# Kernel tuning notes

Measured on AMD Instinct MI355X. Metric: run time of the kernel, lower is better.

## Reference

```python
import jax, jax.numpy as jnp
import numpy as np

N = 100000
E = 3200000
IN_DIM = 500
HID = 64
OUT_DIM = 40
K = 10
ALPHA = 0.1
BN_EPS = 1e-5


def setup_inputs() -> dict:
    key = jax.random.key(0)
    ks = jax.random.split(key, 10)
    x = jax.random.normal(ks[0], (N, IN_DIM), dtype=jnp.float32)
    edge_index = jax.random.randint(ks[1], (2, E), 0, N, dtype=jnp.int64)
    W1 = jax.random.normal(ks[2], (IN_DIM, HID), dtype=jnp.float32) / np.sqrt(IN_DIM)
    b1 = jnp.zeros((HID,), dtype=jnp.float32)
    bn_gamma = jnp.ones((HID,), dtype=jnp.float32)
    bn_beta = jnp.zeros((HID,), dtype=jnp.float32)
    bn_mean = jax.random.normal(ks[3], (HID,), dtype=jnp.float32) * 0.1
    bn_var = jax.random.uniform(ks[4], (HID,), dtype=jnp.float32) + 0.5
    W2 = jax.random.normal(ks[5], (HID, OUT_DIM), dtype=jnp.float32) / np.sqrt(HID)
    b2 = jnp.zeros((OUT_DIM,), dtype=jnp.float32)
    return {"x": x, "edge_index": edge_index, "W1": W1, "b1": b1,
            "bn_gamma": bn_gamma, "bn_beta": bn_beta, "bn_mean": bn_mean,
            "bn_var": bn_var, "W2": W2, "b2": b2}


def _gcn_norm(edge_index):
    # PyG gcn_norm with add_self_loops=True, symmetric normalization.
    row = jnp.concatenate([edge_index[0], jnp.arange(N, dtype=edge_index.dtype)])
    col = jnp.concatenate([edge_index[1], jnp.arange(N, dtype=edge_index.dtype)])
    deg = jax.ops.segment_sum(jnp.ones_like(col, dtype=jnp.float32), col, num_segments=N)
    dinv = jnp.where(deg > 0, jax.lax.rsqrt(deg), 0.0)
    norm = dinv[row] * dinv[col]  # [E+N]
    return row, col, norm


def _appnp(x, row, col, norm):
    h = x
    def step(xk, _):
        msg = norm[:, None] * xk[row]                       # [E+N, HID] gather
        agg = jax.ops.segment_sum(msg, col, num_segments=N)  # scatter-add
        return (1.0 - ALPHA) * agg + ALPHA * h, None
    xK, _ = jax.lax.scan(step, x, None, length=K)
    return xK


def reference(x, edge_index, W1, b1, bn_gamma, bn_beta, bn_mean, bn_var, W2, b2):
    row, col, norm = _gcn_norm(edge_index)
    h = x @ W1 + b1                                   # lin1
    h = _appnp(h, row, col, norm)                     # K-step APPNP
    h = (h - bn_mean) * jax.lax.rsqrt(bn_var + BN_EPS) * bn_gamma + bn_beta  # BN (eval)
    # dropout is identity in eval mode
    emb = h @ W2 + b2                                 # lin2
    out = jax.nn.log_softmax(emb, axis=1)
    return out, emb
```

## Files before the change

kernel.cpp:

```cpp
#include <hip/hip_runtime.h>
#include <math.h>

#define N_NODES 100000
#define N_EDGES 3200000
#define IN_DIM  500
#define HID     64
#define OUT_DIM 40
#define K_ITERS 10
#define ALPHA   0.1f
#define BN_EPS  1e-5f

#define WPAD 48
#define YD   40
#define YH   20
#define NBUCK 782
#define TILE_A 8192
#define APG 48

__device__ __forceinline__ void unpack8(uint4 v, float f[8]) {
    f[0] = __uint_as_float(v.x << 16);
    f[1] = __uint_as_float(v.x & 0xffff0000u);
    f[2] = __uint_as_float(v.y << 16);
    f[3] = __uint_as_float(v.y & 0xffff0000u);
    f[4] = __uint_as_float(v.z << 16);
    f[5] = __uint_as_float(v.z & 0xffff0000u);
    f[6] = __uint_as_float(v.w << 16);
    f[7] = __uint_as_float(v.w & 0xffff0000u);
}
__device__ __forceinline__ unsigned pack2(float a, float b) {
    unsigned ua = __float_as_uint(a);
    unsigned ub = __float_as_uint(b);
    ua += ((ua >> 16) & 1u) + 0x7fffu;
    ub += ((ub >> 16) & 1u) + 0x7fffu;
    return (ua >> 16) | (ub & 0xffff0000u);
}
__device__ __forceinline__ float edge_w(unsigned e) {
    return __uint_as_float((e >> 17) << 16);
}
__device__ __forceinline__ void fma8(float acc[8], float wgt, const float f[8]) {
#pragma unroll
    for (int i = 0; i < 8; ++i) acc[i] = fmaf(wgt, f[i], acc[i]);
}


__global__ void zero_cnt_kernel(int* __restrict__ cnt) {
    int i = blockIdx.x * 256 + threadIdx.x;
    if (i < N_NODES) cnt[i] = 0;
}

__global__ void hist_kernel(const int* __restrict__ ei, int* __restrict__ cnt) {
    int e = blockIdx.x * 256 + threadIdx.x;
    if (e < N_EDGES) atomicAdd(&cnt[ei[N_EDGES + e]], 1);
}

__global__ void reduce_kernel(const int* __restrict__ cnt, int* __restrict__ psum) {
    __shared__ int s[256];
    int i = blockIdx.x * 256 + threadIdx.x;
    int v = (i < N_NODES) ? cnt[i] : 0;
    s[threadIdx.x] = v;
    __syncthreads();
    for (int off = 128; off > 0; off >>= 1) {
        if (threadIdx.x < (unsigned)off) s[threadIdx.x] += s[threadIdx.x + off];
        __syncthreads();
    }
    if (threadIdx.x == 0) psum[blockIdx.x] = s[0];
}

__global__ void scanp_kernel(const int* __restrict__ psum, int* __restrict__ pexcl,
                             int nparts) {
    __shared__ int s[512];
    int t = threadIdx.x;
    int v = (t < nparts) ? psum[t] : 0;
    s[t] = v;
    __syncthreads();
    for (int off = 1; off < 512; off <<= 1) {
        int tv = (t >= off) ? s[t - off] : 0;
        __syncthreads();
        s[t] += tv;
        __syncthreads();
    }
    if (t < nparts) pexcl[t] = s[t] - v;
}

__global__ void apply_kernel(const int* __restrict__ cnt, const int* __restrict__ pexcl,
                             int* __restrict__ rowptr, float* __restrict__ dinv) {
    __shared__ int s[256];
    int t = threadIdx.x;
    int i = blockIdx.x * 256 + t;
    int v = (i < N_NODES) ? cnt[i] : 0;
    s[t] = v;
    __syncthreads();
    for (int off = 1; off < 256; off <<= 1) {
        int tv = (t >= off) ? s[t - off] : 0;
        __syncthreads();
        s[t] += tv;
        __syncthreads();
    }
    if (i < N_NODES) {
        int excl = pexcl[blockIdx.x] + s[t] - v;
        rowptr[i] = excl;
        dinv[i] = rsqrtf((float)(v + 1));
        if (i == N_NODES - 1) rowptr[N_NODES] = excl + v;
    }
}


__global__ void bcur_init_kernel(const int* __restrict__ rowptr, int* __restrict__ bcursor) {
    int i = blockIdx.x * 256 + threadIdx.x;
    if (i < NBUCK) bcursor[i] = rowptr[i << 7];
}

__global__ __launch_bounds__(256) void bucketA_kernel(const int* __restrict__ ei,
                                                      int* __restrict__ bcursor,
                                                      unsigned* __restrict__ ebuf) {
    __shared__ int cnt[NBUCK];
    __shared__ int gbase[NBUCK];
    for (int i = threadIdx.x; i < NBUCK; i += 256) cnt[i] = 0;
    __syncthreads();
    const int e0 = blockIdx.x * TILE_A;
    const int e1 = (e0 + TILE_A < N_EDGES) ? e0 + TILE_A : N_EDGES;
    for (int e = e0 + threadIdx.x; e < e1; e += 256)
        atomicAdd(&cnt[ei[N_EDGES + e] >> 7], 1);
    __syncthreads();
    for (int i = threadIdx.x; i < NBUCK; i += 256) {
        int n = cnt[i];
        gbase[i] = (n > 0) ? atomicAdd(&bcursor[i], n) : 0;
        cnt[i] = 0;
    }
    __syncthreads();
    for (int e = e0 + threadIdx.x; e < e1; e += 256) {
        int r = ei[e];
        int c = ei[N_EDGES + e];
        int b = c >> 7;
        int rank = atomicAdd(&cnt[b], 1);
        ebuf[gbase[b] + rank] = (unsigned)r | ((unsigned)(c & 127) << 17);
    }
}

__global__ __launch_bounds__(256) void bucketB_kernel(const unsigned* __restrict__ ebuf,
                                                      const int* __restrict__ rowptr,
                                                      const float* __restrict__ dinv,
                                                      unsigned* __restrict__ ew) {
    __shared__ int lcur[128];
    __shared__ float ldinv[128];
    const int base = blockIdx.x << 7;
    const int nn = (N_NODES - base < 128) ? (N_NODES - base) : 128;
    if (threadIdx.x < (unsigned)nn) {
        lcur[threadIdx.x] = rowptr[base + threadIdx.x];
        ldinv[threadIdx.x] = dinv[base + threadIdx.x];
    }
    __syncthreads();
    const int s0 = rowptr[base];
    const int hi = (base + 128 < N_NODES) ? base + 128 : N_NODES;
    const int s1 = rowptr[hi];
    for (int p = s0 + threadIdx.x; p < s1; p += 256) {
        unsigned v = ebuf[p];
        int r = v & 0x1ffff;
        int cl = v >> 17;
        int pos = atomicAdd(&lcur[cl], 1);
        float w = dinv[r] * ldinv[cl];
        unsigned f = __float_as_uint(w) + 0x8000u;
        ew[pos] = (unsigned)r | ((f >> 16) << 17);
    }
}

__global__ void prep_kernel(const float* __restrict__ W2, const float* __restrict__ gamma,
                            const float* __restrict__ beta, const float* __restrict__ mean,
                            const float* __restrict__ var, const float* __restrict__ b1,
                            const float* __restrict__ b2, float* __restrict__ W2p,
                            float* __restrict__ c1, float* __restrict__ cbeta) {
    __shared__ float sc[64];
    __shared__ float sd[64];
    int t = threadIdx.x;
    if (t < 64) {
        float s = rsqrtf(var[t] + BN_EPS) * gamma[t];
        sc[t] = s;
        sd[t] = beta[t] - mean[t] * s;
    }
    __syncthreads();
    for (int i = t; i < 64 * OUT_DIM; i += 256) {
        int f = i / OUT_DIM;
        W2p[i] = sc[f] * W2[i];
    }
    if (t < WPAD) {
        if (t < OUT_DIM) {
            float acb = b2[t], ac1 = 0.f;
            for (int f = 0; f < 64; ++f) {
                float w2 = W2[f * OUT_DIM + t];
                acb = fmaf(sd[f], w2, acb);
                ac1 = fmaf(b1[f] * sc[f], w2, ac1);
            }
            cbeta[t] = acb;
            c1[t] = ac1;
        } else {
            c1[t] = 0.f;
        }
    }
}

__global__ __launch_bounds__(256) void wc_kernel(const float* __restrict__ W1,
                                                 const float* __restrict__ W2p,
                                                 float* __restrict__ Wc) {
    __shared__ float w2s[64 * OUT_DIM];
    for (int i = threadIdx.x; i < 64 * OUT_DIM; i += 256) w2s[i] = W2p[i];
    __syncthreads();
    int idx = blockIdx.x * 256 + threadIdx.x;
    if (idx >= IN_DIM * WPAD) return;
    int k = idx / WPAD, o = idx % WPAD;
    float a = 0.f;
    if (o < OUT_DIM) {
        const float* w1r = W1 + (size_t)k * HID;
#pragma unroll 8
        for (int f = 0; f < 64; ++f) a = fmaf(w1r[f], w2s[f * OUT_DIM + o], a);
    }
    Wc[idx] = a;
}

#define L1_M  128
#define L1_KC 20
#define L1_PITCH 132
__global__ __launch_bounds__(256) void lin1_kernel(const float* __restrict__ x,
                                                   const float* __restrict__ Wc,
                                                   const float* __restrict__ c1,
                                                   float* __restrict__ y0f,
                                                   unsigned* __restrict__ y0b) {
    __shared__ float xsT[L1_KC * L1_PITCH];
    __shared__ float wcs[L1_KC * WPAD];

    const int t = threadIdx.x;
    const int ng = t & 31;
    const int og = t >> 5;
    const int nbase = blockIdx.x * L1_M;

    const int srow = t >> 1;
    const int skb  = (t & 1) * 10;
    const int gsrc = nbase + srow;
    const int gcl  = (gsrc < N_NODES) ? gsrc : (N_NODES - 1);
    const float* xrow = x + (size_t)gcl * IN_DIM;

    float acc[4][6];
#pragma unroll
    for (int i = 0; i < 4; ++i)
#pragma unroll
        for (int j = 0; j < 6; ++j) acc[i][j] = 0.0f;

    for (int k0 = 0; k0 < IN_DIM; k0 += L1_KC) {
        __syncthreads();
#pragma unroll
        for (int u = 0; u < 5; ++u) {
            const float2 xv = *(const float2*)(xrow + k0 + skb + 2 * u);
            xsT[(skb + 2 * u) * L1_PITCH + srow]     = xv.x;
            xsT[(skb + 2 * u + 1) * L1_PITCH + srow] = xv.y;
        }
        for (int i = t; i < L1_KC * WPAD; i += 256) wcs[i] = Wc[(size_t)k0 * WPAD + i];
        __syncthreads();

#pragma unroll 4
        for (int k = 0; k < L1_KC; ++k) {
            const float4 xv = *(const float4*)&xsT[k * L1_PITCH + ng * 4];
            float w[6];
#pragma unroll
            for (int j = 0; j < 6; ++j) w[j] = wcs[k * WPAD + og * 6 + j];
            const float xr[4] = {xv.x, xv.y, xv.z, xv.w};
#pragma unroll
            for (int i = 0; i < 4; ++i)
#pragma unroll
                for (int j = 0; j < 6; ++j)
                    acc[i][j] = fmaf(xr[i], w[j], acc[i][j]);
        }
    }

    float cc[6];
#pragma unroll
    for (int j = 0; j < 6; ++j) cc[j] = c1[og * 6 + j];
#pragma unroll
    for (int i = 0; i < 4; ++i) {
        const int n = nbase + ng * 4 + i;
        if (n < N_NODES) {
            float o[6];
#pragma unroll
            for (int j = 0; j < 6; ++j) o[j] = acc[i][j] + cc[j];
            float* yf = y0f + (size_t)n * YD + og * 6;
            unsigned* yb = y0b + (size_t)n * YH + og * 3;
            if (og < 6) {
                *(float2*)(yf)     = make_float2(o[0], o[1]);
                *(float2*)(yf + 2) = make_float2(o[2], o[3]);
                *(float2*)(yf + 4) = make_float2(o[4], o[5]);
                yb[0] = pack2(o[0], o[1]);
                yb[1] = pack2(o[2], o[3]);
                yb[2] = pack2(o[4], o[5]);
            } else if (og == 6) {
                *(float2*)(yf)     = make_float2(o[0], o[1]);
                *(float2*)(yf + 2) = make_float2(o[2], o[3]);
                yb[0] = pack2(o[0], o[1]);
                yb[1] = pack2(o[2], o[3]);
            }
        }
    }
}

template <bool LAST>
__global__ __launch_bounds__(256) void appnp40_kernel(const int* __restrict__ rowptr,
                                                      const unsigned* __restrict__ ew,
                                                      const float* __restrict__ dinv,
                                                      const unsigned* __restrict__ yin,
                                                      const float* __restrict__ h,
                                                      unsigned* __restrict__ yout,
                                                      float* __restrict__ yKf) {
    const int wv   = threadIdx.x >> 6;
    const int lane = threadIdx.x & 63;
    const int sub  = lane / 5;
    const int dl   = lane - sub * 5;
    const int node = blockIdx.x * APG + wv * 12 + sub;
    const bool act = (lane < 60) && (node < N_NODES);
    const int dl4  = dl * 4;

    int beg = 0, end = 0;
    float selfw = 0.f;
    if (act) {
        beg = rowptr[node];
        end = rowptr[node + 1];
        const float di = dinv[node];
        selfw = di * di;
    }

    uint4 vs = make_uint4(0, 0, 0, 0);
    float4 h0 = make_float4(0.f, 0.f, 0.f, 0.f), h1 = h0;
    if (act) {
        vs = *(const uint4*)(yin + (size_t)node * YH + dl4);
        h0 = *(const float4*)(h + (size_t)node * YD + dl * 8);
        h1 = *(const float4*)(h + (size_t)node * YD + dl * 8 + 4);
    }

    float acc[8];
#pragma unroll
    for (int i = 0; i < 8; ++i) acc[i] = 0.f;

    int p = beg;
    for (; p + 3 < end; p += 4) {
        const unsigned e0 = ew[p], e1 = ew[p + 1], e2 = ew[p + 2], e3 = ew[p + 3];
        const uint4 v0 = *(const uint4*)(yin + (size_t)(e0 & 0x1ffff) * YH + dl4);
        const uint4 v1 = *(const uint4*)(yin + (size_t)(e1 & 0x1ffff) * YH + dl4);
        const uint4 v2 = *(const uint4*)(yin + (size_t)(e2 & 0x1ffff) * YH + dl4);
        const uint4 v3 = *(const uint4*)(yin + (size_t)(e3 & 0x1ffff) * YH + dl4);
        float f[8];
        unpack8(v0, f); fma8(acc, edge_w(e0), f);
        unpack8(v1, f); fma8(acc, edge_w(e1), f);
        unpack8(v2, f); fma8(acc, edge_w(e2), f);
        unpack8(v3, f); fma8(acc, edge_w(e3), f);
    }
    for (; p < end; ++p) {
        const unsigned e0 = ew[p];
        const uint4 v0 = *(const uint4*)(yin + (size_t)(e0 & 0x1ffff) * YH + dl4);
        float f[8];
        unpack8(v0, f);
        fma8(acc, edge_w(e0), f);
    }

    if (act) {
        float fs[8];
        unpack8(vs, fs);
        const float ha[8] = {h0.x, h0.y, h0.z, h0.w, h1.x, h1.y, h1.z, h1.w};
        float o[8];
#pragma unroll
        for (int i = 0; i < 8; ++i)
            o[i] = (1.0f - ALPHA) * fmaf(selfw, fs[i], acc[i]) + ALPHA * ha[i];
        if (LAST) {
            *(float4*)(yKf + (size_t)node * YD + dl * 8)     = make_float4(o[0], o[1], o[2], o[3]);
            *(float4*)(yKf + (size_t)node * YD + dl * 8 + 4) = make_float4(o[4], o[5], o[6], o[7]);
        } else {
            uint4 w;
            w.x = pack2(o[0], o[1]);
            w.y = pack2(o[2], o[3]);
            w.z = pack2(o[4], o[5]);
            w.w = pack2(o[6], o[7]);
            *(uint4*)(yout + (size_t)node * YH + dl4) = w;
        }
    }
}

__global__ __launch_bounds__(256) void final_kernel(const float* __restrict__ yKf,
                                                    const float* __restrict__ cbeta,
                                                    float* __restrict__ out_ls,
                                                    float* __restrict__ out_emb) {
    const int lane = threadIdx.x & 63;
    const int wv   = threadIdx.x >> 6;
    const int node = blockIdx.x * 4 + wv;

    float e = 0.0f;
    if (lane < OUT_DIM) e = yKf[(size_t)node * YD + lane] + cbeta[lane];
    float ev = (lane < OUT_DIM) ? e : -INFINITY;
    float m = ev;
#pragma unroll
    for (int off = 32; off > 0; off >>= 1) m = fmaxf(m, __shfl_xor(m, off, 64));
    float p = (lane < OUT_DIM) ? expf(ev - m) : 0.0f;
    float s = p;
#pragma unroll
    for (int off = 32; off > 0; off >>= 1) s += __shfl_xor(s, off, 64);
    if (lane < OUT_DIM) {
        float ls = ev - m - logf(s);
        out_ls[(size_t)node * OUT_DIM + lane] = ls;
        out_emb[(size_t)node * OUT_DIM + lane] = e;
    }
}


extern "C" void kernel_launch(void* const* d_in, const int* in_sizes, int n_in,
                              void* d_out, int out_size, void* d_ws, size_t ws_size,
                              hipStream_t stream) {
    const float* x     = (const float*)d_in[0];
    const int*   ei    = (const int*)d_in[1];
    const float* W1    = (const float*)d_in[2];
    const float* b1    = (const float*)d_in[3];
    const float* gamma = (const float*)d_in[4];
    const float* beta  = (const float*)d_in[5];
    const float* mean  = (const float*)d_in[6];
    const float* var   = (const float*)d_in[7];
    const float* W2    = (const float*)d_in[8];
    const float* b2    = (const float*)d_in[9];

    char* ws = (char*)d_ws;
    size_t off = 0;
    auto alloc = [&](size_t bytes) { char* p = ws + off; off += (bytes + 255) & ~(size_t)255; return p; };

    unsigned* ew     = (unsigned*)alloc((size_t)N_EDGES * 4);
    unsigned* ebuf   = (unsigned*)alloc((size_t)N_EDGES * 4);
    float*    y0f    = (float*)   alloc((size_t)N_NODES * YD * 4);
    float*    yKf    = (float*)   alloc((size_t)N_NODES * YD * 4);
    unsigned* y0b    = (unsigned*)alloc((size_t)N_NODES * YH * 4);
    unsigned* ya     = (unsigned*)alloc((size_t)N_NODES * YH * 4);
    unsigned* yb     = (unsigned*)alloc((size_t)N_NODES * YH * 4);
    float*    Wc     = (float*)   alloc((size_t)IN_DIM * WPAD * 4);
    float*    W2p    = (float*)   alloc(64 * OUT_DIM * 4);
    float*    c1     = (float*)   alloc(WPAD * 4);
    float*    cbeta  = (float*)   alloc(OUT_DIM * 4);
    int*      cnt    = (int*)     alloc(N_NODES * 4);
    float*    dinv   = (float*)   alloc(N_NODES * 4);
    int*      rowptr = (int*)     alloc((N_NODES + 1) * 4);
    int*      bcursor= (int*)     alloc(NBUCK * 4);
    int*      psum   = (int*)     alloc(1600 * 4);
    int*      pexcl  = (int*)     alloc(1600 * 4);

    float* out_ls  = (float*)d_out;
    float* out_emb = (float*)d_out + (size_t)N_NODES * OUT_DIM;

    const int NB_N = (N_NODES + 255) / 256;
    const int NB_E = (N_EDGES + 255) / 256;
    const int NB_A = (N_EDGES + TILE_A - 1) / TILE_A;
    const int NB_P = (N_NODES + APG - 1) / APG;

    zero_cnt_kernel<<<NB_N, 256, 0, stream>>>(cnt);
    hist_kernel<<<NB_E, 256, 0, stream>>>(ei, cnt);
    reduce_kernel<<<NB_N, 256, 0, stream>>>(cnt, psum);
    scanp_kernel<<<1, 512, 0, stream>>>(psum, pexcl, NB_N);
    apply_kernel<<<NB_N, 256, 0, stream>>>(cnt, pexcl, rowptr, dinv);
    bcur_init_kernel<<<(NBUCK + 255) / 256, 256, 0, stream>>>(rowptr, bcursor);
    bucketA_kernel<<<NB_A, 256, 0, stream>>>(ei, bcursor, ebuf);
    bucketB_kernel<<<NBUCK, 256, 0, stream>>>(ebuf, rowptr, dinv, ew);

    prep_kernel<<<1, 256, 0, stream>>>(W2, gamma, beta, mean, var, b1, b2, W2p, c1, cbeta);
    wc_kernel<<<(IN_DIM * WPAD + 255) / 256, 256, 0, stream>>>(W1, W2p, Wc);
    lin1_kernel<<<(N_NODES + L1_M - 1) / L1_M, 256, 0, stream>>>(x, Wc, c1, y0f, y0b);

    const unsigned* cur = y0b;
    unsigned* nxt = ya;
    unsigned* buf[2] = {ya, yb};
    for (int k = 0; k < K_ITERS - 1; ++k) {
        appnp40_kernel<false><<<NB_P, 256, 0, stream>>>(rowptr, ew, dinv, cur,
                                                        y0f, nxt, nullptr);
        cur = nxt;
        nxt = buf[(k + 1) & 1];
    }
    appnp40_kernel<true><<<NB_P, 256, 0, stream>>>(rowptr, ew, dinv, cur,
                                                   y0f, nullptr, yKf);

    final_kernel<<<N_NODES / 4, 256, 0, stream>>>(yKf, cbeta, out_ls, out_emb);
}
```

Measured before the change: 1.318 ms.

## Sort CSR edges by source octant and register-prefetch lin1 tiles

```diff
diff --git a/kernel.cpp b/kernel.cpp
--- a/kernel.cpp
+++ b/kernel.cpp
@@ -16,6 +16,8 @@
 #define NBUCK 782
 #define TILE_A 8192
 #define APG 48
+#define NQ 8
+#define QSHIFT 14
 
 __device__ __forceinline__ void unpack8(uint4 v, float f[8]) {
     f[0] = __uint_as_float(v.x << 16);
@@ -43,20 +45,28 @@
 }
 
 
-__global__ void zero_cnt_kernel(int* __restrict__ cnt) {
+__global__ void zero_cnt_kernel(int* __restrict__ cntq) {
     int i = blockIdx.x * 256 + threadIdx.x;
-    if (i < N_NODES) cnt[i] = 0;
-}
-
-__global__ void hist_kernel(const int* __restrict__ ei, int* __restrict__ cnt) {
+    if (i < NQ * N_NODES) cntq[i] = 0;
+}
+
+__global__ void hist_kernel(const int* __restrict__ ei, int* __restrict__ cntq) {
     int e = blockIdx.x * 256 + threadIdx.x;
-    if (e < N_EDGES) atomicAdd(&cnt[ei[N_EDGES + e]], 1);
-}
-
-__global__ void reduce_kernel(const int* __restrict__ cnt, int* __restrict__ psum) {
+    if (e < N_EDGES) {
+        int r = ei[e];
+        int c = ei[N_EDGES + e];
+        atomicAdd(&cntq[(r >> QSHIFT) * N_NODES + c], 1);
+    }
+}
+
+__global__ void reduce_kernel(const int* __restrict__ cntq, int* __restrict__ psum) {
     __shared__ int s[256];
     int i = blockIdx.x * 256 + threadIdx.x;
-    int v = (i < N_NODES) ? cnt[i] : 0;
+    int v = 0;
+    if (i < N_NODES) {
+#pragma unroll
+        for (int q = 0; q < NQ; ++q) v += cntq[q * N_NODES + i];
+    }
     s[threadIdx.x] = v;
     __syncthreads();
     for (int off = 128; off > 0; off >>= 1) {
@@ -82,12 +92,16 @@
     if (t < nparts) pexcl[t] = s[t] - v;
 }
 
-__global__ void apply_kernel(const int* __restrict__ cnt, const int* __restrict__ pexcl,
+__global__ void apply_kernel(const int* __restrict__ cntq, const int* __restrict__ pexcl,
                              int* __restrict__ rowptr, float* __restrict__ dinv) {
     __shared__ int s[256];
     int t = threadIdx.x;
     int i = blockIdx.x * 256 + t;
-    int v = (i < N_NODES) ? cnt[i] : 0;
+    int v = 0;
+    if (i < N_NODES) {
+#pragma unroll
+        for (int q = 0; q < NQ; ++q) v += cntq[q * N_NODES + i];
+    }
     s[t] = v;
     __syncthreads();
     for (int off = 1; off < 256; off <<= 1) {
@@ -139,15 +153,22 @@
 
 __global__ __launch_bounds__(256) void bucketB_kernel(const unsigned* __restrict__ ebuf,
                                                       const int* __restrict__ rowptr,
+                                                      const int* __restrict__ cntq,
                                                       const float* __restrict__ dinv,
                                                       unsigned* __restrict__ ew) {
-    __shared__ int lcur[128];
+    __shared__ int lcur[NQ * 128];
     __shared__ float ldinv[128];
     const int base = blockIdx.x << 7;
     const int nn = (N_NODES - base < 128) ? (N_NODES - base) : 128;
     if (threadIdx.x < (unsigned)nn) {
-        lcur[threadIdx.x] = rowptr[base + threadIdx.x];
-        ldinv[threadIdx.x] = dinv[base + threadIdx.x];
+        const int gi = base + threadIdx.x;
+        int run = rowptr[gi];
+#pragma unroll
+        for (int q = 0; q < NQ; ++q) {
+            lcur[q * 128 + threadIdx.x] = run;
+            run += cntq[q * N_NODES + gi];
+        }
+        ldinv[threadIdx.x] = dinv[gi];
     }
     __syncthreads();
     const int s0 = rowptr[base];
@@ -157,7 +178,8 @@
         unsigned v = ebuf[p];
         int r = v & 0x1ffff;
         int cl = v >> 17;
-        int pos = atomicAdd(&lcur[cl], 1);
+        int q = r >> QSHIFT;
+        int pos = atomicAdd(&lcur[q * 128 + cl], 1);
         float w = dinv[r] * ldinv[cl];
         unsigned f = __float_as_uint(w) + 0x8000u;
         ew[pos] = (unsigned)r | ((f >> 16) << 17);
@@ -244,16 +266,39 @@
 #pragma unroll
         for (int j = 0; j < 6; ++j) acc[i][j] = 0.0f;
 
+    float2 xr[5];
+    float wr[4];
+#pragma unroll
+    for (int u = 0; u < 5; ++u) xr[u] = *(const float2*)(xrow + skb + 2 * u);
+#pragma unroll
+    for (int j = 0; j < 4; ++j) {
+        int i = t + j * 256;
+        if (i < L1_KC * WPAD) wr[j] = Wc[i];
+    }
+
     for (int k0 = 0; k0 < IN_DIM; k0 += L1_KC) {
-        __syncthreads();
 #pragma unroll
         for (int u = 0; u < 5; ++u) {
-            const float2 xv = *(const float2*)(xrow + k0 + skb + 2 * u);
-            xsT[(skb + 2 * u) * L1_PITCH + srow]     = xv.x;
-            xsT[(skb + 2 * u + 1) * L1_PITCH + srow] = xv.y;
-        }
-        for (int i = t; i < L1_KC * WPAD; i += 256) wcs[i] = Wc[(size_t)k0 * WPAD + i];
-        __syncthreads();
+            xsT[(skb + 2 * u) * L1_PITCH + srow]     = xr[u].x;
+            xsT[(skb + 2 * u + 1) * L1_PITCH + srow] = xr[u].y;
+        }
+#pragma unroll
+        for (int j = 0; j < 4; ++j) {
+            int i = t + j * 256;
+            if (i < L1_KC * WPAD) wcs[i] = wr[j];
+        }
+        __syncthreads();
+
+        const int kn = k0 + L1_KC;
+        if (kn < IN_DIM) {
+#pragma unroll
+            for (int u = 0; u < 5; ++u) xr[u] = *(const float2*)(xrow + kn + skb + 2 * u);
+#pragma unroll
+            for (int j = 0; j < 4; ++j) {
+                int i = t + j * 256;
+                if (i < L1_KC * WPAD) wr[j] = Wc[(size_t)kn * WPAD + i];
+            }
+        }
 
 #pragma unroll 4
         for (int k = 0; k < L1_KC; ++k) {
@@ -261,13 +306,14 @@
             float w[6];
 #pragma unroll
             for (int j = 0; j < 6; ++j) w[j] = wcs[k * WPAD + og * 6 + j];
-            const float xr[4] = {xv.x, xv.y, xv.z, xv.w};
+            const float xr4[4] = {xv.x, xv.y, xv.z, xv.w};
 #pragma unroll
             for (int i = 0; i < 4; ++i)
 #pragma unroll
                 for (int j = 0; j < 6; ++j)
-                    acc[i][j] = fmaf(xr[i], w[j], acc[i][j]);
-        }
+                    acc[i][j] = fmaf(xr4[i], w[j], acc[i][j]);
+        }
+        __syncthreads();
     }
 
     float cc[6];
@@ -434,7 +480,7 @@
     float*    W2p    = (float*)   alloc(64 * OUT_DIM * 4);
     float*    c1     = (float*)   alloc(WPAD * 4);
     float*    cbeta  = (float*)   alloc(OUT_DIM * 4);
-    int*      cnt    = (int*)     alloc(N_NODES * 4);
+    int*      cntq   = (int*)     alloc((size_t)NQ * N_NODES * 4);
     float*    dinv   = (float*)   alloc(N_NODES * 4);
     int*      rowptr = (int*)     alloc((N_NODES + 1) * 4);
     int*      bcursor= (int*)     alloc(NBUCK * 4);
@@ -448,15 +494,16 @@
     const int NB_E = (N_EDGES + 255) / 256;
     const int NB_A = (N_EDGES + TILE_A - 1) / TILE_A;
     const int NB_P = (N_NODES + APG - 1) / APG;
-
-    zero_cnt_kernel<<<NB_N, 256, 0, stream>>>(cnt);
-    hist_kernel<<<NB_E, 256, 0, stream>>>(ei, cnt);
-    reduce_kernel<<<NB_N, 256, 0, stream>>>(cnt, psum);
+    const int NB_Z = (NQ * N_NODES + 255) / 256;
+
+    zero_cnt_kernel<<<NB_Z, 256, 0, stream>>>(cntq);
+    hist_kernel<<<NB_E, 256, 0, stream>>>(ei, cntq);
+    reduce_kernel<<<NB_N, 256, 0, stream>>>(cntq, psum);
     scanp_kernel<<<1, 512, 0, stream>>>(psum, pexcl, NB_N);
-    apply_kernel<<<NB_N, 256, 0, stream>>>(cnt, pexcl, rowptr, dinv);
+    apply_kernel<<<NB_N, 256, 0, stream>>>(cntq, pexcl, rowptr, dinv);
     bcur_init_kernel<<<(NBUCK + 255) / 256, 256, 0, stream>>>(rowptr, bcursor);
     bucketA_kernel<<<NB_A, 256, 0, stream>>>(ei, bcursor, ebuf);
-    bucketB_kernel<<<NBUCK, 256, 0, stream>>>(ebuf, rowptr, dinv, ew);
+    bucketB_kernel<<<NBUCK, 256, 0, stream>>>(ebuf, rowptr, cntq, dinv, ew);
 
     prep_kernel<<<1, 256, 0, stream>>>(W2, gamma, beta, mean, var, b1, b2, W2p, c1, cbeta);
     wc_kernel<<<(IN_DIM * WPAD + 255) / 256, 256, 0, stream>>>(W1, W2p, Wc);
```

Result: faster. 1.171 ms (-11.2%).
